# Kernel tuning notes

Measured on AMD Instinct MI355X. Metric: run time of the kernel, lower is better.

## Reference

```python
import jax, jax.numpy as jnp
import numpy as np


def setup_inputs() -> dict:
    key = jax.random.key(0)
    k1, k2 = jax.random.split(key)
    x = jax.random.normal(k1, (64, 64, 64, 64), dtype=jnp.float32)
    embeddings = jax.random.normal(k2, (400, 64), dtype=jnp.float32) * 0.1
    return {"x": x, "embeddings": embeddings}


def reference(x, embeddings):
    D = embeddings.shape[1]
    flat_x = x.reshape(-1, D)  # [N, D]
    # squared L2 distance via sum-of-squares + matmul: [N, K]
    distances = (
        jnp.sum(flat_x * flat_x, axis=1, keepdims=True)
        + jnp.sum(embeddings * embeddings, axis=1)
        - 2.0 * jnp.matmul(flat_x, embeddings.T)
    )
    encoding_indices = jnp.argmin(distances, axis=1)  # [N]
    quantized = jnp.take(embeddings, encoding_indices, axis=0)  # [N, D]
    return quantized.reshape(x.shape)
```

## Files before the change

### kernel.cpp

```cpp
#include <hip/hip_runtime.h>

#define D 64
#define K 400
#define KT 25
#define BLOCK 1024
#define WPB (BLOCK / 64)

typedef _Float16 f16x8 __attribute__((ext_vector_type(8)));
typedef float f32x4 __attribute__((ext_vector_type(4)));

__global__ __launch_bounds__(BLOCK, 4) void vq_mfma(
    const float* __restrict__ x,
    const float* __restrict__ emb,
    float* __restrict__ out,
    int nrows) {
  __shared__ __align__(16) _Float16 sB[KT][4][64][8];
  __shared__ float s_norm[K];

  const int tid = threadIdx.x;

  for (int e = tid; e < KT * 4 * 64; e += BLOCK) {
    int t = e >> 8;
    int f = (e >> 6) & 3;
    int l = e & 63;
    int code = t * 16 + (l & 15);
    int kb = ((l >> 4) << 3) + ((f >> 1) << 5);
    const float* ep = emb + code * D + kb;
    float v[8];
    *(float4*)&v[0] = *(const float4*)ep;
    *(float4*)&v[4] = *(const float4*)(ep + 4);
    _Float16 h[8];
    if ((f & 1) == 0) {
#pragma unroll
      for (int j = 0; j < 8; ++j) h[j] = (_Float16)(2.0f * v[j]);
    } else {
#pragma unroll
      for (int j = 0; j < 8; ++j) {
        float s = 2.0f * v[j];
        _Float16 hh = (_Float16)s;
        float r = s - (float)hh;
        h[j] = (_Float16)(r * 2048.0f);
      }
    }
    *(f16x8*)&sB[t][f][l][0] = *(f16x8*)&h[0];
  }
  for (int k = tid; k < K; k += BLOCK) {
    const float4* ep = (const float4*)(emb + (size_t)k * D);
    float4 s4 = {0.f, 0.f, 0.f, 0.f};
#pragma unroll
    for (int d = 0; d < 16; ++d) {
      float4 v = ep[d];
      s4.x = fmaf(v.x, v.x, s4.x);
      s4.y = fmaf(v.y, v.y, s4.y);
      s4.z = fmaf(v.z, v.z, s4.z);
      s4.w = fmaf(v.w, v.w, s4.w);
    }
    s_norm[k] = (s4.x + s4.y) + (s4.z + s4.w);
  }
  __syncthreads();

  const int lane = tid & 63;
  const int wid = tid >> 6;
  const int gw = blockIdx.x * WPB + wid;
  const int nw = gridDim.x * WPB;
  const int l15 = lane & 15;
  const int q = lane >> 4;

#define LOADB(Bf, Nf, T)                           \
  do {                                             \
    Bf##0 = *(const f16x8*)&sB[(T)][0][lane][0];   \
    Bf##1 = *(const f16x8*)&sB[(T)][1][lane][0];   \
    Bf##2 = *(const f16x8*)&sB[(T)][2][lane][0];   \
    Bf##3 = *(const f16x8*)&sB[(T)][3][lane][0];   \
    Nf = s_norm[(T) * 16 + l15];                   \
  } while (0)

#define PROC(Bf, Nf, T)                                                        \
  do {                                                                         \
    const float nn_ = -(Nf);                                                   \
    _Pragma("unroll") for (int a_ = 0; a_ < 2; ++a_) {                         \
      f32x4 ah = {nn_, nn_, nn_, nn_};                                         \
      f32x4 al = {0.f, 0.f, 0.f, 0.f};                                         \
      ah = __builtin_amdgcn_mfma_f32_16x16x32_f16(xh[a_][0], Bf##0, ah, 0, 0, 0); \
      ah = __builtin_amdgcn_mfma_f32_16x16x32_f16(xh[a_][1], Bf##2, ah, 0, 0, 0); \
      al = __builtin_amdgcn_mfma_f32_16x16x32_f16(xh[a_][0], Bf##1, al, 0, 0, 0); \
      al = __builtin_amdgcn_mfma_f32_16x16x32_f16(xl[a_][0], Bf##0, al, 0, 0, 0); \
      al = __builtin_amdgcn_mfma_f32_16x16x32_f16(xh[a_][1], Bf##3, al, 0, 0, 0); \
      al = __builtin_amdgcn_mfma_f32_16x16x32_f16(xl[a_][1], Bf##2, al, 0, 0, 0); \
      _Pragma("unroll") for (int i_ = 0; i_ < 4; ++i_) {                       \
        float m_ = fmaf(al[i_], 4.8828125e-4f, ah[i_]);  \
        bool gt_ = m_ > bestm[a_][i_];                                         \
        bestm[a_][i_] = gt_ ? m_ : bestm[a_][i_];                              \
        bestt[a_][i_] = gt_ ? (T) : bestt[a_][i_];                             \
      }                                                                        \
    }                                                                          \
  } while (0)

  const int npair = nrows >> 5;
  for (int p = gw; p < npair; p += nw) {
    const int row0 = p << 5;

    f16x8 xh[2][2], xl[2][2];
#pragma unroll
    for (int a = 0; a < 2; ++a)
#pragma unroll
      for (int c = 0; c < 2; ++c) {
        const float* xp =
            x + (size_t)(row0 + a * 16 + l15) * D + q * 8 + c * 32;
        float v[8];
        *(float4*)&v[0] = *(const float4*)xp;
        *(float4*)&v[4] = *(const float4*)(xp + 4);
        _Float16 hh[8], ll[8];
#pragma unroll
        for (int j = 0; j < 8; ++j) {
          _Float16 h = (_Float16)v[j];
          float r = v[j] - (float)h;
          hh[j] = h;
          ll[j] = (_Float16)(r * 2048.0f);
        }
        xh[a][c] = *(f16x8*)&hh[0];
        xl[a][c] = *(f16x8*)&ll[0];
      }

    float bestm[2][4];
    int bestt[2][4];
#pragma unroll
    for (int a = 0; a < 2; ++a)
#pragma unroll
      for (int i = 0; i < 4; ++i) {
        bestm[a][i] = -3.4e38f;
        bestt[a][i] = 0;
      }

    f16x8 bA0, bA1, bA2, bA3, bB0, bB1, bB2, bB3;
    float nA, nB;
    LOADB(bA, nA, 0);
    for (int t2 = 0; t2 < 12; ++t2) {
      LOADB(bB, nB, 2 * t2 + 1);
      PROC(bA, nA, 2 * t2);
      LOADB(bA, nA, 2 * t2 + 2);
      PROC(bB, nB, 2 * t2 + 1);
    }
    PROC(bA, nA, 24);

#pragma unroll
    for (int a = 0; a < 2; ++a) {
      float bv[4];
      int bk[4];
#pragma unroll
      for (int i = 0; i < 4; ++i) {
        bv[i] = bestm[a][i];
        bk[i] = bestt[a][i] * 16 + l15;
      }
#pragma unroll
      for (int m = 1; m <= 8; m <<= 1) {
#pragma unroll
        for (int i = 0; i < 4; ++i) {
          float ov = __shfl_xor(bv[i], m, 64);
          int ok = __shfl_xor(bk[i], m, 64);
          bool take = (ov > bv[i]) || ((ov == bv[i]) && (ok < bk[i]));
          bv[i] = take ? ov : bv[i];
          bk[i] = take ? ok : bk[i];
        }
      }
      int j = (lane >> 2) & 3;
      int k01 = (j & 1) ? bk[1] : bk[0];
      int k23 = (j & 1) ? bk[3] : bk[2];
      int kk = (j & 2) ? k23 : k01;
      int r = row0 + a * 16 + (lane >> 2);
      const f32x4* src = (const f32x4*)(emb + (size_t)kk * D);
      f32x4* dst = (f32x4*)(out + (size_t)r * D);
#pragma unroll
      for (int s = 0; s < 4; ++s) {
        int idx = (lane & 3) + (s << 2);
        f32x4 v = src[idx];
        __builtin_nontemporal_store(v, &dst[idx]);
      }
    }
  }
#undef LOADB
#undef PROC
}

extern "C" void kernel_launch(void* const* d_in, const int* in_sizes, int n_in,
                              void* d_out, int out_size, void* d_ws, size_t ws_size,
                              hipStream_t stream) {
  const float* x = (const float*)d_in[0];
  const float* emb = (const float*)d_in[1];
  float* out = (float*)d_out;
  int nrows = in_sizes[0] / D;
  vq_mfma<<<256, BLOCK, 0, stream>>>(x, emb, out, nrows);
}
```

Before: 148.5 us.

## Prefetch next row tile into registers and tune MFMA scheduling priority

Software-prefetches the next iteration's x rows into registers so global load latency overlaps the current tile's MFMA work. Other changes: the MFMA chains now start from a zero accumulator and the code norm is subtracted afterwards, s_setprio is raised around the MFMA groups, and sched_barriers are added. The shuffle reductions for both row halves are interleaved, and the nontemporal output stores become plain stores. Costs are extra register pressure at 4 blocks per SM, one extra VALU subtract per element, and possible cache pollution from the normal stores.

```diff
diff --git a/kernel.cpp b/kernel.cpp
--- a/kernel.cpp
+++ b/kernel.cpp
@@ -66,6 +66,8 @@
   const int l15 = lane & 15;
   const int q = lane >> 4;
 
+  const f32x4 zq = {0.f, 0.f, 0.f, 0.f};
+
 #define LOADB(Bf, Nf, T)                           \
   do {                                             \
     Bf##0 = *(const f16x8*)&sB[(T)][0][lane][0];   \
@@ -73,22 +75,23 @@
     Bf##2 = *(const f16x8*)&sB[(T)][2][lane][0];   \
     Bf##3 = *(const f16x8*)&sB[(T)][3][lane][0];   \
     Nf = s_norm[(T) * 16 + l15];                   \
+    __builtin_amdgcn_sched_barrier(0);             \
   } while (0)
 
 #define PROC(Bf, Nf, T)                                                        \
   do {                                                                         \
-    const float nn_ = -(Nf);                                                   \
     _Pragma("unroll") for (int a_ = 0; a_ < 2; ++a_) {                         \
-      f32x4 ah = {nn_, nn_, nn_, nn_};                                         \
-      f32x4 al = {0.f, 0.f, 0.f, 0.f};                                         \
-      ah = __builtin_amdgcn_mfma_f32_16x16x32_f16(xh[a_][0], Bf##0, ah, 0, 0, 0); \
+      f32x4 ah, al;                                                            \
+      __builtin_amdgcn_s_setprio(1);                                           \
+      ah = __builtin_amdgcn_mfma_f32_16x16x32_f16(xh[a_][0], Bf##0, zq, 0, 0, 0); \
       ah = __builtin_amdgcn_mfma_f32_16x16x32_f16(xh[a_][1], Bf##2, ah, 0, 0, 0); \
-      al = __builtin_amdgcn_mfma_f32_16x16x32_f16(xh[a_][0], Bf##1, al, 0, 0, 0); \
+      al = __builtin_amdgcn_mfma_f32_16x16x32_f16(xh[a_][0], Bf##1, zq, 0, 0, 0); \
       al = __builtin_amdgcn_mfma_f32_16x16x32_f16(xl[a_][0], Bf##0, al, 0, 0, 0); \
       al = __builtin_amdgcn_mfma_f32_16x16x32_f16(xh[a_][1], Bf##3, al, 0, 0, 0); \
       al = __builtin_amdgcn_mfma_f32_16x16x32_f16(xl[a_][1], Bf##2, al, 0, 0, 0); \
+      __builtin_amdgcn_s_setprio(0);                                           \
       _Pragma("unroll") for (int i_ = 0; i_ < 4; ++i_) {                       \
-        float m_ = fmaf(al[i_], 4.8828125e-4f, ah[i_]);  \
+        float m_ = fmaf(al[i_], 4.8828125e-4f, ah[i_]) - (Nf);                 \
         bool gt_ = m_ > bestm[a_][i_];                                         \
         bestm[a_][i_] = gt_ ? m_ : bestm[a_][i_];                              \
         bestt[a_][i_] = gt_ ? (T) : bestt[a_][i_];                             \
@@ -97,6 +100,21 @@
   } while (0)
 
   const int npair = nrows >> 5;
+
+  float4 pv[2][2][2];
+  int p0 = gw;
+  if (p0 < npair) {
+#pragma unroll
+    for (int a = 0; a < 2; ++a)
+#pragma unroll
+      for (int c = 0; c < 2; ++c) {
+        const float* xp =
+            x + (size_t)((p0 << 5) + a * 16 + l15) * D + q * 8 + c * 32;
+        pv[a][c][0] = *(const float4*)xp;
+        pv[a][c][1] = *(const float4*)(xp + 4);
+      }
+  }
+
   for (int p = gw; p < npair; p += nw) {
     const int row0 = p << 5;
 
@@ -105,11 +123,9 @@
     for (int a = 0; a < 2; ++a)
 #pragma unroll
       for (int c = 0; c < 2; ++c) {
-        const float* xp =
-            x + (size_t)(row0 + a * 16 + l15) * D + q * 8 + c * 32;
         float v[8];
-        *(float4*)&v[0] = *(const float4*)xp;
-        *(float4*)&v[4] = *(const float4*)(xp + 4);
+        *(float4*)&v[0] = pv[a][c][0];
+        *(float4*)&v[4] = pv[a][c][1];
         _Float16 hh[8], ll[8];
 #pragma unroll
         for (int j = 0; j < 8; ++j) {
@@ -122,6 +138,22 @@
         xl[a][c] = *(f16x8*)&ll[0];
       }
 
+    {
+      int pn = p + nw;
+      if (pn < npair) {
+#pragma unroll
+        for (int a = 0; a < 2; ++a)
+#pragma unroll
+          for (int c = 0; c < 2; ++c) {
+            const float* xp =
+                x + (size_t)((pn << 5) + a * 16 + l15) * D + q * 8 + c * 32;
+            pv[a][c][0] = *(const float4*)xp;
+            pv[a][c][1] = *(const float4*)(xp + 4);
+          }
+        __builtin_amdgcn_sched_barrier(0);
+      }
+    }
+
     float bestm[2][4];
     int bestt[2][4];
 #pragma unroll
@@ -143,29 +175,33 @@
     }
     PROC(bA, nA, 24);
 
+    float bv[2][4];
+    int bk[2][4];
+#pragma unroll
+    for (int a = 0; a < 2; ++a)
+#pragma unroll
+      for (int i = 0; i < 4; ++i) {
+        bv[a][i] = bestm[a][i];
+        bk[a][i] = bestt[a][i] * 16 + l15;
+      }
+#pragma unroll
+    for (int m = 1; m <= 8; m <<= 1) {
+#pragma unroll
+      for (int a = 0; a < 2; ++a)
+#pragma unroll
+        for (int i = 0; i < 4; ++i) {
+          float ov = __shfl_xor(bv[a][i], m, 64);
+          int ok = __shfl_xor(bk[a][i], m, 64);
+          bool take = (ov > bv[a][i]) || ((ov == bv[a][i]) && (ok < bk[a][i]));
+          bv[a][i] = take ? ov : bv[a][i];
+          bk[a][i] = take ? ok : bk[a][i];
+        }
+    }
 #pragma unroll
     for (int a = 0; a < 2; ++a) {
-      float bv[4];
-      int bk[4];
-#pragma unroll
-      for (int i = 0; i < 4; ++i) {
-        bv[i] = bestm[a][i];
-        bk[i] = bestt[a][i] * 16 + l15;
-      }
-#pragma unroll
-      for (int m = 1; m <= 8; m <<= 1) {
-#pragma unroll
-        for (int i = 0; i < 4; ++i) {
-          float ov = __shfl_xor(bv[i], m, 64);
-          int ok = __shfl_xor(bk[i], m, 64);
-          bool take = (ov > bv[i]) || ((ov == bv[i]) && (ok < bk[i]));
-          bv[i] = take ? ov : bv[i];
-          bk[i] = take ? ok : bk[i];
-        }
-      }
       int j = (lane >> 2) & 3;
-      int k01 = (j & 1) ? bk[1] : bk[0];
-      int k23 = (j & 1) ? bk[3] : bk[2];
+      int k01 = (j & 1) ? bk[a][1] : bk[a][0];
+      int k23 = (j & 1) ? bk[a][3] : bk[a][2];
       int kk = (j & 2) ? k23 : k01;
       int r = row0 + a * 16 + (lane >> 2);
       const f32x4* src = (const f32x4*)(emb + (size_t)kk * D);
@@ -173,8 +209,7 @@
 #pragma unroll
       for (int s = 0; s < 4; ++s) {
         int idx = (lane & 3) + (s << 2);
-        f32x4 v = src[idx];
-        __builtin_nontemporal_store(v, &dst[idx]);
+        dst[idx] = src[idx];
       }
     }
   }
```

New measurement: 177.0 us. +19.1%, slower.
